# Performance work log

Hardware: AMD Instinct MI355X
Metric: run time of the kernel (lower is better)

## Reference

```python
import jax, jax.numpy as jnp
import numpy as np

K = 5            # local_window_size
S = K * K + 1    # num_affinity_samples = 26


def _local_indices(H, W, k):
    # Mirrors generate_local_indices: reflection-pad an arange index map and
    # unfold kxk windows -> [H*W, k*k] flat node indices.
    p = (k - 1) // 2
    idx = np.arange(H * W, dtype=np.int64).reshape(H, W)
    idx = np.pad(idx, p, mode='reflect')
    win = np.lib.stride_tricks.sliding_window_view(idx, (k, k))  # [H,W,k,k]
    return win.reshape(H * W, k * k)


def setup_inputs() -> dict:
    key = jax.random.key(0)
    ks = jax.random.split(key, 8)
    B, C, H, W = 4, 64, 128, 128
    D = 64  # kq_dim
    s = 1.0 / np.sqrt(C)
    return {
        'x': jax.random.normal(ks[0], (B, C, H, W), jnp.float32),
        'conv_w': jax.random.normal(ks[1], (D, C), jnp.float32) * s,
        'conv_b': jax.random.normal(ks[2], (D,), jnp.float32) * 0.01,
        'key_w': jax.random.normal(ks[3], (D, D), jnp.float32) * s,
        'key_b': jax.random.normal(ks[4], (D,), jnp.float32) * 0.01,
        'query_w': jax.random.normal(ks[5], (D, D), jnp.float32) * s,
        'query_b': jax.random.normal(ks[6], (D,), jnp.float32) * 0.01,
        'rand_global_inds': jax.random.randint(ks[7], (B, H * W, S - K * K), 0, H * W).astype(jnp.int64),
    }


def reference(x, conv_w, conv_b, key_w, key_b, query_w, query_b, rand_global_inds):
    B, C, H, W = x.shape
    HW = H * W
    # 1x1 conv (kq_conv): [B,C,H,W] -> [B,H,W,D]
    kq = jnp.einsum('bchw,dc->bhwd', x, conv_w) + conv_b
    # keys/query decoders (torch Linear: y = x W^T + b), flattened to [B,HW,D]
    keys = (kq @ key_w.T + key_b).reshape(B, HW, -1)
    queries = (kq @ query_w.T + query_b).reshape(B, HW, -1)
    # sample indices: 25 local window neighbors + 1 random global per node
    local = jnp.asarray(_local_indices(H, W, K))                 # [HW, 25]
    local = jnp.broadcast_to(local[None], (B, HW, K * K))
    sample_inds = jnp.concatenate([local, rand_global_inds], -1)  # [B,HW,S]
    # gather keys at sampled indices: [B,HW,S,D]
    gathered_key = jax.vmap(lambda k, idx: k[idx])(keys, sample_inds)
    # per-sample dot product with the node's own query, scaled by C^-0.5
    logits = jnp.einsum('bnd,bnsd->bns', queries, gathered_key) * (C ** -0.5)
    return logits
```

## Files before the change

### kernel.cpp

```cpp
#include <hip/hip_runtime.h>
#include <hip/hip_bf16.h>

#define HW 16384
#define NB 4

typedef __attribute__((ext_vector_type(8))) short bf16x8;
typedef __attribute__((ext_vector_type(4))) float f32x4;

__device__ __forceinline__ float blo(unsigned u) { return __uint_as_float(u << 16); }
__device__ __forceinline__ float bhi(unsigned u) { return __uint_as_float(u & 0xffff0000u); }


__global__ __launch_bounds__(256) void combine_weights(
    const float* __restrict__ conv_w, const float* __restrict__ conv_b,
    const float* __restrict__ key_w, const float* __restrict__ key_b,
    const float* __restrict__ query_w, const float* __restrict__ query_b,
    ushort* __restrict__ Wb, float* __restrict__ bout) {
    int t = threadIdx.x, bx = blockIdx.x;
    int sel = bx >> 4, d0 = (bx & 15) * 4;
    const float* Wm = sel ? query_w : key_w;
    int dd = t >> 6, c = t & 63;
    const float* wrow = Wm + (d0 + dd) * 64;
    float acc = 0.f;
    #pragma unroll
    for (int k = 0; k < 64; ++k) acc = fmaf(wrow[k], conv_w[k * 64 + c], acc);
    __hip_bfloat16 h = __float2bfloat16(acc);
    Wb[(sel * 64 + d0 + dd) * 64 + c] = *(ushort*)&h;
    if (t < 4) {
        const float* wr2 = Wm + (d0 + t) * 64;
        float bacc = 0.f;
        #pragma unroll
        for (int k = 0; k < 64; ++k) bacc = fmaf(wr2[k], conv_b[k], bacc);
        bacc += (sel ? query_b : key_b)[d0 + t];
        bout[sel * 64 + d0 + t] = bacc;
    }
}

__global__ __launch_bounds__(256) void gemm_kq(
    const float* __restrict__ x, const ushort* __restrict__ W,
    const float* __restrict__ bias, ushort* __restrict__ keys,
    ushort* __restrict__ queries) {
    __shared__ ushort xs[64 * 64];
    __shared__ ushort epi[64 * 64];
    __shared__ float bs[128];
    int t = threadIdx.x;
    int b = blockIdx.x >> 8;
    int n0 = (blockIdx.x & 255) << 6;

    if (t < 128) bs[t] = bias[t];
    {
        int r = t & 63, q0 = t >> 6;
        const float* xp = x + ((size_t)(b * 64 + q0 * 16)) * HW + n0 + r;
        unsigned u[8];
        #pragma unroll
        for (int cc = 0; cc < 8; ++cc) {
            float lo = xp[(size_t)(2 * cc) * HW];
            float hi = xp[(size_t)(2 * cc + 1) * HW];
            __hip_bfloat162 h2 = __float22bfloat162_rn(make_float2(lo, hi));
            u[cc] = *(unsigned*)&h2;
        }
        #pragma unroll
        for (int q = 0; q < 2; ++q) {
            int qq = q0 * 2 + q;
            *(uint4*)((char*)xs + r * 128 + ((qq ^ (r & 7)) << 4)) =
                make_uint4(u[4 * q], u[4 * q + 1], u[4 * q + 2], u[4 * q + 3]);
        }
    }
    __syncthreads();

    int l = t & 63, w = t >> 6;
    int ncol = l & 15, kg = l >> 4;

    bf16x8 Bf[2];
    int brow = w * 16 + ncol;
    #pragma unroll
    for (int half = 0; half < 2; ++half)
        Bf[half] = *(bf16x8*)((char*)xs + brow * 128 + (((half * 4 + kg) ^ (brow & 7)) << 4));

    f32x4 acc[8];
    #pragma unroll
    for (int dt = 0; dt < 8; ++dt) acc[dt] = (f32x4){0.f, 0.f, 0.f, 0.f};

    #pragma unroll
    for (int dt = 0; dt < 8; ++dt) {
        const bf16x8* arow = (const bf16x8*)(W + (dt * 16 + ncol) * 64 + kg * 8);
        acc[dt] = __builtin_amdgcn_mfma_f32_16x16x32_bf16(arow[0], Bf[0], acc[dt], 0, 0, 0);
        acc[dt] = __builtin_amdgcn_mfma_f32_16x16x32_bf16(arow[4], Bf[1], acc[dt], 0, 0, 0);
    }

    #pragma unroll
    for (int p = 0; p < 2; ++p) {
        #pragma unroll
        for (int dt = 0; dt < 4; ++dt) {
            int dbase = dt * 16 + kg * 4;
            float4 bb = *(float4*)&bs[p * 64 + dbase];
            int n = w * 16 + ncol;
            f32x4 a = acc[p * 4 + dt];
            __hip_bfloat162 lo2 = __float22bfloat162_rn(make_float2(a[0] + bb.x, a[1] + bb.y));
            __hip_bfloat162 hi2 = __float22bfloat162_rn(make_float2(a[2] + bb.z, a[3] + bb.w));
            *(uint2*)((char*)epi + n * 128 + (((dbase >> 3) ^ (n & 7)) << 4) + ((dbase & 4) << 1)) =
                make_uint2(*(unsigned*)&lo2, *(unsigned*)&hi2);
        }
        __syncthreads();
        ushort* dst = p ? queries : keys;
        #pragma unroll
        for (int i = 0; i < 2; ++i) {
            int idx = i * 256 + t;
            int row = idx >> 3, ch = idx & 7;
            uint4 v = *(uint4*)((char*)epi + row * 128 + ((ch ^ (row & 7)) << 4));
            *(uint4*)(dst + (((size_t)(b * HW + n0 + row)) << 6) + ch * 8) = v;
        }
        __syncthreads();
    }
}

#define DOT(s_, idxn_) do {                                                   \
    const uint4* kp = (const uint4*)(kb_ + ((size_t)(idxn_) << 6));           \
    uint4 ka = kp[0], kc = kp[1];                                             \
    float a = 0.f;                                                            \
    a = fmaf(blo(ka.x), qf[0], a);  a = fmaf(bhi(ka.x), qf[1], a);            \
    a = fmaf(blo(ka.y), qf[2], a);  a = fmaf(bhi(ka.y), qf[3], a);            \
    a = fmaf(blo(ka.z), qf[4], a);  a = fmaf(bhi(ka.z), qf[5], a);            \
    a = fmaf(blo(ka.w), qf[6], a);  a = fmaf(bhi(ka.w), qf[7], a);            \
    a = fmaf(blo(kc.x), qf[8], a);  a = fmaf(bhi(kc.x), qf[9], a);            \
    a = fmaf(blo(kc.y), qf[10], a); a = fmaf(bhi(kc.y), qf[11], a);           \
    a = fmaf(blo(kc.z), qf[12], a); a = fmaf(bhi(kc.z), qf[13], a);           \
    a = fmaf(blo(kc.w), qf[14], a); a = fmaf(bhi(kc.w), qf[15], a);           \
    a += __shfl_xor(a, 1);                                                    \
    a += __shfl_xor(a, 2);                                                    \
    if (j == 0) res[n_loc * 26 + (s_)] = a * 0.125f;                          \
} while (0)

#define SAMP(s_, dy_, dx_) do {                                               \
    int ry = y + (dy_);                                                       \
    if ((dy_) < 0) ry = (ry < 0) ? -ry : ry;                                  \
    if ((dy_) > 0) ry = (ry > 127) ? 254 - ry : ry;                           \
    int rx = xq + (dx_);                                                      \
    if ((dx_) < 0) rx = (rx < 0) ? -rx : rx;                                  \
    if ((dx_) > 0) rx = (rx > 127) ? 254 - rx : rx;                           \
    DOT(s_, (ry << 7) + rx);                                                  \
} while (0)

__global__ __launch_bounds__(256) void affinity(
    const ushort* __restrict__ keys, const ushort* __restrict__ queries,
    const int* __restrict__ rnd, float* __restrict__ out) {
    __shared__ float res[416];
    int t = threadIdx.x;
    int b = blockIdx.x >> 10;
    int n0 = (blockIdx.x & 1023) << 4;

    int j = t & 3;
    int g = t >> 2;
    int n_loc = g & 15;
    int sb = g >> 4;
    int n = n0 + n_loc;

    const uint4* qp = (const uint4*)(queries + (((size_t)(b * HW + n)) << 6) + j * 16);
    uint4 qa = qp[0], qb = qp[1];
    float qf[16];
    qf[0] = blo(qa.x); qf[1] = bhi(qa.x); qf[2] = blo(qa.y); qf[3] = bhi(qa.y);
    qf[4] = blo(qa.z); qf[5] = bhi(qa.z); qf[6] = blo(qa.w); qf[7] = bhi(qa.w);
    qf[8] = blo(qb.x); qf[9] = bhi(qb.x); qf[10] = blo(qb.y); qf[11] = bhi(qb.y);
    qf[12] = blo(qb.z); qf[13] = bhi(qb.z); qf[14] = blo(qb.w); qf[15] = bhi(qb.w);

    int y = n >> 7, xq = n & 127;
    const ushort* kb_ = keys + (((size_t)b * HW) << 6) + j * 16;

    switch (sb) {
    case 0:
        SAMP(0, -2, -2); SAMP(4, -2, 2);  SAMP(8, -1, 1);  SAMP(12, 0, 0);
        SAMP(16, 1, -1); SAMP(20, 2, -2); SAMP(24, 2, 2);
        break;
    case 1: {
        SAMP(1, -2, -1); SAMP(5, -1, -2); SAMP(9, -1, 2);  SAMP(13, 0, 1);
        SAMP(17, 1, 0);  SAMP(21, 2, -1);
        int rix = rnd[b * HW + n];
        DOT(25, rix);
        break;
    }
    case 2:
        SAMP(2, -2, 0);  SAMP(6, -1, -1); SAMP(10, 0, -2); SAMP(14, 0, 2);
        SAMP(18, 1, 1);  SAMP(22, 2, 0);
        break;
    default:
        SAMP(3, -2, 1);  SAMP(7, -1, 0);  SAMP(11, 0, -1); SAMP(15, 1, -2);
        SAMP(19, 1, 2);  SAMP(23, 2, 1);
        break;
    }
    __syncthreads();
    size_t ob = ((size_t)(b * HW + n0)) * 26;
    out[ob + t] = res[t];
    if (t < 160) out[ob + 256 + t] = res[256 + t];
}

extern "C" void kernel_launch(void* const* d_in, const int* in_sizes, int n_in,
                              void* d_out, int out_size, void* d_ws, size_t ws_size,
                              hipStream_t stream) {
    const float* x       = (const float*)d_in[0];
    const float* conv_w  = (const float*)d_in[1];
    const float* conv_b  = (const float*)d_in[2];
    const float* key_w   = (const float*)d_in[3];
    const float* key_b   = (const float*)d_in[4];
    const float* query_w = (const float*)d_in[5];
    const float* query_b = (const float*)d_in[6];
    const int*   rnd     = (const int*)d_in[7];
    float* out = (float*)d_out;

    ushort* Wb    = (ushort*)d_ws;
    float*  biasp = (float*)((char*)d_ws + 16384);
    ushort* keys  = (ushort*)((char*)d_ws + 32768);
    ushort* quer  = keys + (size_t)NB * HW * 64;

    combine_weights<<<32, 256, 0, stream>>>(conv_w, conv_b, key_w, key_b,
                                            query_w, query_b, Wb, biasp);
    gemm_kq<<<NB * (HW / 64), 256, 0, stream>>>(x, Wb, biasp, keys, quer);
    affinity<<<NB * (HW / 16), 256, 0, stream>>>(keys, quer, rnd, out);
}
```

Measured before the change: 38.71 us.

## Fuse query projection into affinity kernel, keeping queries in shared memory

The GEMM kernel now computes only keys. The affinity kernel recomputes queries for its 64-node tile from x, using MFMA, and keeps them in LDS, so the query tensor is never written to or read back from global memory. Each thread now handles all 26 samples for one node instead of splitting the samples across four thread groups. The cost is a second full read of x, more serial work per thread, and fewer affinity blocks.

```diff
diff --git a/kernel.cpp b/kernel.cpp
--- a/kernel.cpp
+++ b/kernel.cpp
@@ -36,36 +36,38 @@
     }
 }
 
-__global__ __launch_bounds__(256) void gemm_kq(
+__device__ __forceinline__ void stage_x(const float* __restrict__ x, ushort* xs,
+                                        int b, int n0, int t) {
+    int r = t & 63, q0 = t >> 6;
+    const float* xp = x + ((size_t)(b * 64 + q0 * 16)) * HW + n0 + r;
+    unsigned u[8];
+    #pragma unroll
+    for (int cc = 0; cc < 8; ++cc) {
+        float lo = xp[(size_t)(2 * cc) * HW];
+        float hi = xp[(size_t)(2 * cc + 1) * HW];
+        __hip_bfloat162 h2 = __float22bfloat162_rn(make_float2(lo, hi));
+        u[cc] = *(unsigned*)&h2;
+    }
+    #pragma unroll
+    for (int qq = 0; qq < 2; ++qq) {
+        int c16 = q0 * 2 + qq;
+        *(uint4*)((char*)xs + r * 128 + ((c16 ^ (r & 7)) << 4)) =
+            make_uint4(u[4 * qq], u[4 * qq + 1], u[4 * qq + 2], u[4 * qq + 3]);
+    }
+}
+
+__global__ __launch_bounds__(256) void gemm_keys(
     const float* __restrict__ x, const ushort* __restrict__ W,
-    const float* __restrict__ bias, ushort* __restrict__ keys,
-    ushort* __restrict__ queries) {
+    const float* __restrict__ bias, ushort* __restrict__ keys) {
     __shared__ ushort xs[64 * 64];
     __shared__ ushort epi[64 * 64];
-    __shared__ float bs[128];
+    __shared__ float bs[64];
     int t = threadIdx.x;
     int b = blockIdx.x >> 8;
     int n0 = (blockIdx.x & 255) << 6;
 
-    if (t < 128) bs[t] = bias[t];
-    {
-        int r = t & 63, q0 = t >> 6;
-        const float* xp = x + ((size_t)(b * 64 + q0 * 16)) * HW + n0 + r;
-        unsigned u[8];
-        #pragma unroll
-        for (int cc = 0; cc < 8; ++cc) {
-            float lo = xp[(size_t)(2 * cc) * HW];
-            float hi = xp[(size_t)(2 * cc + 1) * HW];
-            __hip_bfloat162 h2 = __float22bfloat162_rn(make_float2(lo, hi));
-            u[cc] = *(unsigned*)&h2;
-        }
-        #pragma unroll
-        for (int q = 0; q < 2; ++q) {
-            int qq = q0 * 2 + q;
-            *(uint4*)((char*)xs + r * 128 + ((qq ^ (r & 7)) << 4)) =
-                make_uint4(u[4 * q], u[4 * q + 1], u[4 * q + 2], u[4 * q + 3]);
-        }
-    }
+    if (t < 64) bs[t] = bias[t];
+    stage_x(x, xs, b, n0, t);
     __syncthreads();
 
     int l = t & 63, w = t >> 6;
@@ -77,40 +79,34 @@
     for (int half = 0; half < 2; ++half)
         Bf[half] = *(bf16x8*)((char*)xs + brow * 128 + (((half * 4 + kg) ^ (brow & 7)) << 4));
 
-    f32x4 acc[8];
-    #pragma unroll
-    for (int dt = 0; dt < 8; ++dt) acc[dt] = (f32x4){0.f, 0.f, 0.f, 0.f};
-
-    #pragma unroll
-    for (int dt = 0; dt < 8; ++dt) {
+    f32x4 acc[4];
+    #pragma unroll
+    for (int dt = 0; dt < 4; ++dt) acc[dt] = (f32x4){0.f, 0.f, 0.f, 0.f};
+    #pragma unroll
+    for (int dt = 0; dt < 4; ++dt) {
         const bf16x8* arow = (const bf16x8*)(W + (dt * 16 + ncol) * 64 + kg * 8);
         acc[dt] = __builtin_amdgcn_mfma_f32_16x16x32_bf16(arow[0], Bf[0], acc[dt], 0, 0, 0);
         acc[dt] = __builtin_amdgcn_mfma_f32_16x16x32_bf16(arow[4], Bf[1], acc[dt], 0, 0, 0);
     }
 
     #pragma unroll
-    for (int p = 0; p < 2; ++p) {
-        #pragma unroll
-        for (int dt = 0; dt < 4; ++dt) {
-            int dbase = dt * 16 + kg * 4;
-            float4 bb = *(float4*)&bs[p * 64 + dbase];
-            int n = w * 16 + ncol;
-            f32x4 a = acc[p * 4 + dt];
-            __hip_bfloat162 lo2 = __float22bfloat162_rn(make_float2(a[0] + bb.x, a[1] + bb.y));
-            __hip_bfloat162 hi2 = __float22bfloat162_rn(make_float2(a[2] + bb.z, a[3] + bb.w));
-            *(uint2*)((char*)epi + n * 128 + (((dbase >> 3) ^ (n & 7)) << 4) + ((dbase & 4) << 1)) =
-                make_uint2(*(unsigned*)&lo2, *(unsigned*)&hi2);
-        }
-        __syncthreads();
-        ushort* dst = p ? queries : keys;
-        #pragma unroll
-        for (int i = 0; i < 2; ++i) {
-            int idx = i * 256 + t;
-            int row = idx >> 3, ch = idx & 7;
-            uint4 v = *(uint4*)((char*)epi + row * 128 + ((ch ^ (row & 7)) << 4));
-            *(uint4*)(dst + (((size_t)(b * HW + n0 + row)) << 6) + ch * 8) = v;
-        }
-        __syncthreads();
+    for (int dt = 0; dt < 4; ++dt) {
+        int dbase = dt * 16 + kg * 4;
+        float4 bb = *(float4*)&bs[dbase];
+        int nl = w * 16 + ncol;
+        f32x4 a = acc[dt];
+        __hip_bfloat162 lo2 = __float22bfloat162_rn(make_float2(a[0] + bb.x, a[1] + bb.y));
+        __hip_bfloat162 hi2 = __float22bfloat162_rn(make_float2(a[2] + bb.z, a[3] + bb.w));
+        *(uint2*)((char*)epi + nl * 128 + (((dbase >> 3) ^ (nl & 7)) << 4) + ((dbase & 4) << 1)) =
+            make_uint2(*(unsigned*)&lo2, *(unsigned*)&hi2);
+    }
+    __syncthreads();
+    #pragma unroll
+    for (int i = 0; i < 2; ++i) {
+        int idx = i * 256 + t;
+        int row = idx >> 3, ch = idx & 7;
+        uint4 v = *(uint4*)((char*)epi + row * 128 + ((ch ^ (row & 7)) << 4));
+        *(uint4*)(keys + (((size_t)(b * HW + n0 + row)) << 6) + ch * 8) = v;
     }
 }
 
@@ -141,56 +137,84 @@
     DOT(s_, (ry << 7) + rx);                                                  \
 } while (0)
 
-__global__ __launch_bounds__(256) void affinity(
-    const ushort* __restrict__ keys, const ushort* __restrict__ queries,
+__global__ __launch_bounds__(256) void query_affinity(
+    const float* __restrict__ x, const ushort* __restrict__ W,
+    const float* __restrict__ bias, const ushort* __restrict__ keys,
     const int* __restrict__ rnd, float* __restrict__ out) {
-    __shared__ float res[416];
+    __shared__ ushort xs[64 * 64];
+    __shared__ ushort qs[64 * 64];
+    __shared__ float bs[64];
     int t = threadIdx.x;
-    int b = blockIdx.x >> 10;
-    int n0 = (blockIdx.x & 1023) << 4;
-
+    int b = blockIdx.x >> 8;
+    int n0 = (blockIdx.x & 255) << 6;
+
+    if (t < 64) bs[t] = bias[64 + t];
+    stage_x(x, xs, b, n0, t);
+    __syncthreads();
+
+    int l = t & 63, w = t >> 6;
+    int ncol = l & 15, kg = l >> 4;
+
+    bf16x8 Bf[2];
+    int brow = w * 16 + ncol;
+    #pragma unroll
+    for (int half = 0; half < 2; ++half)
+        Bf[half] = *(bf16x8*)((char*)xs + brow * 128 + (((half * 4 + kg) ^ (brow & 7)) << 4));
+
+    f32x4 acc[4];
+    #pragma unroll
+    for (int dt = 0; dt < 4; ++dt) acc[dt] = (f32x4){0.f, 0.f, 0.f, 0.f};
+    #pragma unroll
+    for (int dt = 0; dt < 4; ++dt) {
+        const bf16x8* arow = (const bf16x8*)(W + (64 + dt * 16 + ncol) * 64 + kg * 8);
+        acc[dt] = __builtin_amdgcn_mfma_f32_16x16x32_bf16(arow[0], Bf[0], acc[dt], 0, 0, 0);
+        acc[dt] = __builtin_amdgcn_mfma_f32_16x16x32_bf16(arow[4], Bf[1], acc[dt], 0, 0, 0);
+    }
+
+    #pragma unroll
+    for (int dt = 0; dt < 4; ++dt) {
+        int dbase = dt * 16 + kg * 4;
+        float4 bb = *(float4*)&bs[dbase];
+        int nl = w * 16 + ncol;
+        f32x4 a = acc[dt];
+        __hip_bfloat162 lo2 = __float22bfloat162_rn(make_float2(a[0] + bb.x, a[1] + bb.y));
+        __hip_bfloat162 hi2 = __float22bfloat162_rn(make_float2(a[2] + bb.z, a[3] + bb.w));
+        *(uint2*)((char*)qs + nl * 128 + (((dbase >> 3) ^ (nl & 7)) << 4) + ((dbase & 4) << 1)) =
+            make_uint2(*(unsigned*)&lo2, *(unsigned*)&hi2);
+    }
+    __syncthreads();
+
+    float* res = (float*)xs;
     int j = t & 3;
-    int g = t >> 2;
-    int n_loc = g & 15;
-    int sb = g >> 4;
-    int n = n0 + n_loc;
-
-    const uint4* qp = (const uint4*)(queries + (((size_t)(b * HW + n)) << 6) + j * 16);
-    uint4 qa = qp[0], qb = qp[1];
+    int n_loc = t >> 2;
+    uint4 qa = *(uint4*)((char*)qs + n_loc * 128 + (((2 * j) ^ (n_loc & 7)) << 4));
+    uint4 qb = *(uint4*)((char*)qs + n_loc * 128 + (((2 * j + 1) ^ (n_loc & 7)) << 4));
     float qf[16];
     qf[0] = blo(qa.x); qf[1] = bhi(qa.x); qf[2] = blo(qa.y); qf[3] = bhi(qa.y);
     qf[4] = blo(qa.z); qf[5] = bhi(qa.z); qf[6] = blo(qa.w); qf[7] = bhi(qa.w);
     qf[8] = blo(qb.x); qf[9] = bhi(qb.x); qf[10] = blo(qb.y); qf[11] = bhi(qb.y);
     qf[12] = blo(qb.z); qf[13] = bhi(qb.z); qf[14] = blo(qb.w); qf[15] = bhi(qb.w);
 
+    int n = n0 + n_loc;
     int y = n >> 7, xq = n & 127;
     const ushort* kb_ = keys + (((size_t)b * HW) << 6) + j * 16;
-
-    switch (sb) {
-    case 0:
-        SAMP(0, -2, -2); SAMP(4, -2, 2);  SAMP(8, -1, 1);  SAMP(12, 0, 0);
-        SAMP(16, 1, -1); SAMP(20, 2, -2); SAMP(24, 2, 2);
-        break;
-    case 1: {
-        SAMP(1, -2, -1); SAMP(5, -1, -2); SAMP(9, -1, 2);  SAMP(13, 0, 1);
-        SAMP(17, 1, 0);  SAMP(21, 2, -1);
-        int rix = rnd[b * HW + n];
-        DOT(25, rix);
-        break;
-    }
-    case 2:
-        SAMP(2, -2, 0);  SAMP(6, -1, -1); SAMP(10, 0, -2); SAMP(14, 0, 2);
-        SAMP(18, 1, 1);  SAMP(22, 2, 0);
-        break;
-    default:
-        SAMP(3, -2, 1);  SAMP(7, -1, 0);  SAMP(11, 0, -1); SAMP(15, 1, -2);
-        SAMP(19, 1, 2);  SAMP(23, 2, 1);
-        break;
-    }
+    int rix = rnd[b * HW + n];
+
+    SAMP(0, -2, -2);  SAMP(1, -2, -1);  SAMP(2, -2, 0);   SAMP(3, -2, 1);
+    SAMP(4, -2, 2);   SAMP(5, -1, -2);  SAMP(6, -1, -1);  SAMP(7, -1, 0);
+    SAMP(8, -1, 1);   SAMP(9, -1, 2);   SAMP(10, 0, -2);  SAMP(11, 0, -1);
+    SAMP(12, 0, 0);   SAMP(13, 0, 1);   SAMP(14, 0, 2);   SAMP(15, 1, -2);
+    SAMP(16, 1, -1);  SAMP(17, 1, 0);   SAMP(18, 1, 1);   SAMP(19, 1, 2);
+    SAMP(20, 2, -2);  SAMP(21, 2, -1);  SAMP(22, 2, 0);   SAMP(23, 2, 1);
+    SAMP(24, 2, 2);   DOT(25, rix);
+
     __syncthreads();
     size_t ob = ((size_t)(b * HW + n0)) * 26;
-    out[ob + t] = res[t];
-    if (t < 160) out[ob + 256 + t] = res[256 + t];
+    #pragma unroll
+    for (int i = 0; i < 7; ++i) {
+        int idx = i * 256 + t;
+        if (idx < 1664) out[ob + idx] = res[idx];
+    }
 }
 
 extern "C" void kernel_launch(void* const* d_in, const int* in_sizes, int n_in,
@@ -209,10 +233,9 @@
     ushort* Wb    = (ushort*)d_ws;
     float*  biasp = (float*)((char*)d_ws + 16384);
     ushort* keys  = (ushort*)((char*)d_ws + 32768);
-    ushort* quer  = keys + (size_t)NB * HW * 64;
 
     combine_weights<<<32, 256, 0, stream>>>(conv_w, conv_b, key_w, key_b,
                                             query_w, query_b, Wb, biasp);
-    gemm_kq<<<NB * (HW / 64), 256, 0, stream>>>(x, Wb, biasp, keys, quer);
-    affinity<<<NB * (HW / 16), 256, 0, stream>>>(keys, quer, rnd, out);
-}
+    gemm_keys<<<NB * (HW / 64), 256, 0, stream>>>(x, Wb, biasp, keys);
+    query_affinity<<<NB * (HW / 64), 256, 0, stream>>>(x, Wb, biasp, keys, rnd, out);
+}
```

Result: slower. 42.20 us (+9.0%).

## Enlarge GEMM tile to 128 pixels, vectorize x loads, fold scale into query weights

Applied to the files above, without the earlier changes.

The kq GEMM now processes 128 pixels per block instead of 64. Each wave computes a 64x64 output tile from register-held B fragments, and both key and query outputs are written through a single doubled epilogue buffer with one sync. The x tile is loaded with float4 reads along the pixel dimension rather than scalar strided reads. The C^-0.5 scale is folded into the combined query weights and bias, which removes a multiply per sample in the affinity kernel. The larger tile uses more LDS and registers and halves the block count, which may lower occupancy; scaling before the bf16 rounding also changes rounding slightly.

```diff
diff --git a/kernel.cpp b/kernel.cpp
--- a/kernel.cpp
+++ b/kernel.cpp
@@ -19,12 +19,13 @@
     int t = threadIdx.x, bx = blockIdx.x;
     int sel = bx >> 4, d0 = (bx & 15) * 4;
     const float* Wm = sel ? query_w : key_w;
+    float scale = sel ? 0.125f : 1.0f;
     int dd = t >> 6, c = t & 63;
     const float* wrow = Wm + (d0 + dd) * 64;
     float acc = 0.f;
     #pragma unroll
     for (int k = 0; k < 64; ++k) acc = fmaf(wrow[k], conv_w[k * 64 + c], acc);
-    __hip_bfloat16 h = __float2bfloat16(acc);
+    __hip_bfloat16 h = __float2bfloat16(acc * scale);
     Wb[(sel * 64 + d0 + dd) * 64 + c] = *(ushort*)&h;
     if (t < 4) {
         const float* wr2 = Wm + (d0 + t) * 64;
@@ -32,7 +33,7 @@
         #pragma unroll
         for (int k = 0; k < 64; ++k) bacc = fmaf(wr2[k], conv_b[k], bacc);
         bacc += (sel ? query_b : key_b)[d0 + t];
-        bout[sel * 64 + d0 + t] = bacc;
+        bout[sel * 64 + d0 + t] = bacc * scale;
     }
 }
 
@@ -40,77 +41,93 @@
     const float* __restrict__ x, const ushort* __restrict__ W,
     const float* __restrict__ bias, ushort* __restrict__ keys,
     ushort* __restrict__ queries) {
-    __shared__ ushort xs[64 * 64];
-    __shared__ ushort epi[64 * 64];
+    __shared__ ushort xs[128 * 64];
+    __shared__ ushort epi[2 * 128 * 64];
     __shared__ float bs[128];
     int t = threadIdx.x;
-    int b = blockIdx.x >> 8;
-    int n0 = (blockIdx.x & 255) << 6;
+    int b = blockIdx.x >> 7;
+    int n0 = (blockIdx.x & 127) << 7;
 
     if (t < 128) bs[t] = bias[t];
     {
-        int r = t & 63, q0 = t >> 6;
-        const float* xp = x + ((size_t)(b * 64 + q0 * 16)) * HW + n0 + r;
-        unsigned u[8];
-        #pragma unroll
-        for (int cc = 0; cc < 8; ++cc) {
-            float lo = xp[(size_t)(2 * cc) * HW];
-            float hi = xp[(size_t)(2 * cc + 1) * HW];
-            __hip_bfloat162 h2 = __float22bfloat162_rn(make_float2(lo, hi));
-            u[cc] = *(unsigned*)&h2;
-        }
-        #pragma unroll
-        for (int q = 0; q < 2; ++q) {
-            int qq = q0 * 2 + q;
-            *(uint4*)((char*)xs + r * 128 + ((qq ^ (r & 7)) << 4)) =
-                make_uint4(u[4 * q], u[4 * q + 1], u[4 * q + 2], u[4 * q + 3]);
+        int c0 = (t >> 5) * 8, nb = (t & 31) * 4;
+        const float* xp = x + ((size_t)(b * 64 + c0)) * HW + n0 + nb;
+        float4 v[8];
+        #pragma unroll
+        for (int r = 0; r < 8; ++r) v[r] = *(const float4*)(xp + (size_t)r * HW);
+        int chunk = c0 >> 3;
+        #pragma unroll
+        for (int nn = 0; nn < 4; ++nn) {
+            unsigned u[4];
+            #pragma unroll
+            for (int cc = 0; cc < 4; ++cc) {
+                float lo = ((const float*)&v[2 * cc])[nn];
+                float hi = ((const float*)&v[2 * cc + 1])[nn];
+                __hip_bfloat162 h2 = __float22bfloat162_rn(make_float2(lo, hi));
+                u[cc] = *(unsigned*)&h2;
+            }
+            int row = nb + nn;
+            *(uint4*)((char*)xs + row * 128 + ((chunk ^ (row & 7)) << 4)) =
+                make_uint4(u[0], u[1], u[2], u[3]);
         }
     }
     __syncthreads();
 
     int l = t & 63, w = t >> 6;
     int ncol = l & 15, kg = l >> 4;
-
-    bf16x8 Bf[2];
-    int brow = w * 16 + ncol;
-    #pragma unroll
-    for (int half = 0; half < 2; ++half)
-        Bf[half] = *(bf16x8*)((char*)xs + brow * 128 + (((half * 4 + kg) ^ (brow & 7)) << 4));
-
-    f32x4 acc[8];
-    #pragma unroll
-    for (int dt = 0; dt < 8; ++dt) acc[dt] = (f32x4){0.f, 0.f, 0.f, 0.f};
-
-    #pragma unroll
-    for (int dt = 0; dt < 8; ++dt) {
-        const bf16x8* arow = (const bf16x8*)(W + (dt * 16 + ncol) * 64 + kg * 8);
-        acc[dt] = __builtin_amdgcn_mfma_f32_16x16x32_bf16(arow[0], Bf[0], acc[dt], 0, 0, 0);
-        acc[dt] = __builtin_amdgcn_mfma_f32_16x16x32_bf16(arow[4], Bf[1], acc[dt], 0, 0, 0);
-    }
-
-    #pragma unroll
-    for (int p = 0; p < 2; ++p) {
-        #pragma unroll
-        for (int dt = 0; dt < 4; ++dt) {
-            int dbase = dt * 16 + kg * 4;
-            float4 bb = *(float4*)&bs[p * 64 + dbase];
-            int n = w * 16 + ncol;
-            f32x4 a = acc[p * 4 + dt];
+    int nhalf = w & 1, dhalf = w >> 1;
+
+    bf16x8 Bf[4][2];
+    #pragma unroll
+    for (int nt = 0; nt < 4; ++nt) {
+        int row = nhalf * 64 + nt * 16 + ncol;
+        #pragma unroll
+        for (int half = 0; half < 2; ++half)
+            Bf[nt][half] = *(bf16x8*)((char*)xs + row * 128 + (((half * 4 + kg) ^ (row & 7)) << 4));
+    }
+
+    f32x4 acc[4][4];
+    #pragma unroll
+    for (int dt = 0; dt < 4; ++dt)
+        #pragma unroll
+        for (int nt = 0; nt < 4; ++nt) acc[dt][nt] = (f32x4){0.f, 0.f, 0.f, 0.f};
+
+    #pragma unroll
+    for (int dt = 0; dt < 4; ++dt) {
+        const bf16x8* arow = (const bf16x8*)(W + ((dhalf * 64 + dt * 16 + ncol)) * 64 + kg * 8);
+        bf16x8 A0 = arow[0];
+        bf16x8 A1 = arow[4];
+        #pragma unroll
+        for (int nt = 0; nt < 4; ++nt) {
+            acc[dt][nt] = __builtin_amdgcn_mfma_f32_16x16x32_bf16(A0, Bf[nt][0], acc[dt][nt], 0, 0, 0);
+            acc[dt][nt] = __builtin_amdgcn_mfma_f32_16x16x32_bf16(A1, Bf[nt][1], acc[dt][nt], 0, 0, 0);
+        }
+    }
+
+    #pragma unroll
+    for (int dt = 0; dt < 4; ++dt) {
+        int dbase = dt * 16 + kg * 4;
+        float4 bb = *(float4*)&bs[dhalf * 64 + dbase];
+        #pragma unroll
+        for (int nt = 0; nt < 4; ++nt) {
+            int nl = nhalf * 64 + nt * 16 + ncol;
+            f32x4 a = acc[dt][nt];
             __hip_bfloat162 lo2 = __float22bfloat162_rn(make_float2(a[0] + bb.x, a[1] + bb.y));
             __hip_bfloat162 hi2 = __float22bfloat162_rn(make_float2(a[2] + bb.z, a[3] + bb.w));
-            *(uint2*)((char*)epi + n * 128 + (((dbase >> 3) ^ (n & 7)) << 4) + ((dbase & 4) << 1)) =
+            *(uint2*)((char*)epi + dhalf * 16384 + nl * 128 +
+                      (((dbase >> 3) ^ (nl & 7)) << 4) + ((dbase & 4) << 1)) =
                 make_uint2(*(unsigned*)&lo2, *(unsigned*)&hi2);
         }
-        __syncthreads();
-        ushort* dst = p ? queries : keys;
-        #pragma unroll
-        for (int i = 0; i < 2; ++i) {
-            int idx = i * 256 + t;
-            int row = idx >> 3, ch = idx & 7;
-            uint4 v = *(uint4*)((char*)epi + row * 128 + ((ch ^ (row & 7)) << 4));
-            *(uint4*)(dst + (((size_t)(b * HW + n0 + row)) << 6) + ch * 8) = v;
-        }
-        __syncthreads();
+    }
+    __syncthreads();
+    #pragma unroll
+    for (int i = 0; i < 8; ++i) {
+        int u = i * 256 + t;
+        int arr = u >> 10;
+        int row = (u >> 3) & 127, ch = u & 7;
+        uint4 v = *(uint4*)((char*)epi + arr * 16384 + row * 128 + ((ch ^ (row & 7)) << 4));
+        ushort* dst = arr ? queries : keys;
+        *(uint4*)(dst + (((size_t)(b * HW + n0 + row)) << 6) + ch * 8) = v;
     }
 }
 
@@ -128,7 +145,7 @@
     a = fmaf(blo(kc.w), qf[14], a); a = fmaf(bhi(kc.w), qf[15], a);           \
     a += __shfl_xor(a, 1);                                                    \
     a += __shfl_xor(a, 2);                                                    \
-    if (j == 0) res[n_loc * 26 + (s_)] = a * 0.125f;                          \
+    if (j == 0) res[n_loc * 26 + (s_)] = a;                                   \
 } while (0)
 
 #define SAMP(s_, dy_, dx_) do {                                               \
@@ -213,6 +230,6 @@
 
     combine_weights<<<32, 256, 0, stream>>>(conv_w, conv_b, key_w, key_b,
                                             query_w, query_b, Wb, biasp);
-    gemm_kq<<<NB * (HW / 64), 256, 0, stream>>>(x, Wb, biasp, keys, quer);
+    gemm_kq<<<NB * (HW / 128), 256, 0, stream>>>(x, Wb, biasp, keys, quer);
     affinity<<<NB * (HW / 16), 256, 0, stream>>>(keys, quer, rnd, out);
 }
```

Measured after the change: 34.42 us. 1.12x faster.
